# Kernel optimization log

Hardware: AMD Instinct MI355X
Metric: run time of the kernel (lower is better)

## Reference

```python
import jax, jax.numpy as jnp
import numpy as np

B, S, D, C = 64, 576, 768, 200


def setup_inputs() -> dict:
    key = jax.random.key(0)
    k1, k2, k3, k4 = jax.random.split(key, 4)
    return {
        "patch_tokens": jax.random.normal(k1, (B, S, D), dtype=jnp.float32),
        "class_token": jax.random.normal(k2, (B, D), dtype=jnp.float32),
        "attn_w": jax.random.normal(k3, (C, D), dtype=jnp.float32) * (1.0 / np.sqrt(D)),
        "attn_b": jnp.zeros((C,), dtype=jnp.float32),
        "gc_w": jax.random.normal(k4, (C, D), dtype=jnp.float32) * (1.0 / np.sqrt(D)),
        "gc_b": jnp.zeros((C,), dtype=jnp.float32),
        "lam": jnp.ones((1,), dtype=jnp.float32),
    }


def reference(patch_tokens, class_token, attn_w, attn_b, gc_w, gc_b, lam):
    # patch_tokens: (B,S,D). The torch module reshapes S to HxW, but the mean
    # over (H,W) equals the mean over S, so we stay in token layout.
    _, S_, D_ = patch_tokens.shape
    # Global classifier: (B,C)
    global_scores = class_token @ gc_w.T + gc_b
    # Per-class 1x1 conv == per-class linear projection over tokens: (B,C,S)
    att = jax.nn.sigmoid(
        jnp.einsum("bsd,cd->bcs", patch_tokens, attn_w) + attn_b[None, :, None]
    )
    # mean over spatial (S) then mean over channels (D):
    # mean_d mean_s (att * feat) == einsum / (S*D)
    attention_scores = jnp.einsum("bcs,bsd->bc", att, patch_tokens) / (S_ * D_)
    return global_scores + lam[0] * attention_scores
```

## Files before the change

kernel.cpp:

```cpp
#include <hip/hip_runtime.h>
#include <math.h>

#define Bsz  64
#define Ssz  576
#define Dsz  768
#define Csz  200
#define NPAD 208
#define MT   48
#define BK   64
#define NKT  12

typedef float f32x4 __attribute__((ext_vector_type(4)));

#define AS_GLOBAL __attribute__((address_space(1)))
#define AS_LDS    __attribute__((address_space(3)))

__device__ inline void gload16(const void* g, void* l) {
    __builtin_amdgcn_global_load_lds((const AS_GLOBAL unsigned int*)g,
                                     (AS_LDS unsigned int*)l, 16, 0, 0);
}

__global__ __launch_bounds__(256) void prep_w8(const float* __restrict__ W,
                                               unsigned int* __restrict__ Wq) {
    const int i   = blockIdx.x * 256 + threadIdx.x;
    const int row = i / 192;
    const int col = (i % 192) * 4;
    unsigned int w = 0;
    if (row < Csz) {
        const float4 v = *(const float4*)(W + (size_t)row * Dsz + col);
        w = __builtin_amdgcn_cvt_pk_fp8_f32(v.x, v.y, 0u, false);
        w = __builtin_amdgcn_cvt_pk_fp8_f32(v.z, v.w, w, true);
    } else if (row == Csz) {
        w = 0x38383838u;
    }
    Wq[i] = w;
}

__global__ __launch_bounds__(256) void gc_kernel(
    const float* __restrict__ ct, const float* __restrict__ gw,
    const float* __restrict__ gb, float* __restrict__ out) {
    const int b    = blockIdx.x;
    const int wv   = threadIdx.x >> 6;
    const int lane = threadIdx.x & 63;
    const int c    = blockIdx.y * 4 + wv;
    const float* wr = gw + (size_t)c * Dsz + lane * 12;
    const float* cr = ct + (size_t)b * Dsz + lane * 12;
    float s = 0.f;
#pragma unroll
    for (int j = 0; j < 3; ++j) {
        const float4 w = *(const float4*)(wr + 4 * j);
        const float4 x = *(const float4*)(cr + 4 * j);
        s += w.x * x.x + w.y * x.y + w.z * x.z + w.w * x.w;
    }
#pragma unroll
    for (int off = 32; off > 0; off >>= 1) s += __shfl_down(s, off, 64);
    if (lane == 0) out[b * Csz + c] = s + gb[c];
}

__global__ __launch_bounds__(256, 3) void attn_kernel(
    const float* __restrict__ X,
    const unsigned char* __restrict__ Wq,
    const float* __restrict__ attn_b,
    const float* __restrict__ lam,
    float* __restrict__ out)
{
    __shared__ float         sX[2][MT * BK];
    __shared__ unsigned char sW[2][NPAD * BK];

    const int tid  = threadIdx.x;
    const int lane = tid & 63;
    const int w    = tid >> 6;
    const int m    = lane & 15;
    const int q    = lane >> 4;
    const int rowbase = blockIdx.x * MT;
    const int bidx    = blockIdx.x / 12;

    const float* xg[3];
    int xsl[3];
#pragma unroll
    for (int j = 0; j < 3; ++j) {
        const int g    = 3 * w + j;
        const int xrow = g * 4 + (lane >> 4);
        const int xgc  = (lane & 15) ^ (xrow & 15);
        xg[j]  = X + (size_t)(rowbase + xrow) * Dsz + xgc * 4;
        xsl[j] = g * 64;
    }

    const int wng = (w < 3) ? 3 : 4;
    const int wg0 = 3 * w;
    const unsigned char* wgp = Wq + (size_t)(lane >> 2) * Dsz
                                  + (((lane & 3) ^ ((lane >> 2) & 3)) * 16);

    f32x4 acc[13];
#pragma unroll
    for (int t = 0; t < 13; ++t) acc[t] = (f32x4){0.f, 0.f, 0.f, 0.f};

    const int rA   = w * 16 + m;
    const int akey = rA & 15;
    const int bkey = m & 3;

#pragma unroll
    for (int j = 0; j < 3; ++j)
        gload16(xg[j], &sX[0][xsl[j] * 4]);
#pragma unroll
    for (int j = 0; j < 4; ++j)
        if (j < wng) gload16(wgp + (size_t)(wg0 + j) * 16 * Dsz, &sW[0][(wg0 + j) * 1024]);

    for (int kt = 0; kt < NKT; ++kt) {
        const int p = kt & 1;
        __syncthreads();
        if (kt + 1 < NKT) {
            const int kx = (kt + 1) * BK;
#pragma unroll
            for (int j = 0; j < 3; ++j)
                gload16(xg[j] + kx, &sX[p ^ 1][xsl[j] * 4]);
#pragma unroll
            for (int j = 0; j < 4; ++j)
                if (j < wng) gload16(wgp + (size_t)(wg0 + j) * 16 * Dsz + kx,
                                     &sW[p ^ 1][(wg0 + j) * 1024]);
        }
        if (w < 3) {
#pragma unroll
            for (int k2 = 0; k2 < 2; ++k2) {
                const int c0 = k2 * 8 + 2 * q;
                const float4 alo = *(const float4*)&sX[p][rA * 64 + ((c0) ^ akey) * 4];
                const float4 ahi = *(const float4*)&sX[p][rA * 64 + ((c0 + 1) ^ akey) * 4];
                union { long l; unsigned int u[2]; } A;
                A.u[0] = __builtin_amdgcn_cvt_pk_fp8_f32(alo.x, alo.y, 0u, false);
                A.u[0] = __builtin_amdgcn_cvt_pk_fp8_f32(alo.z, alo.w, A.u[0], true);
                A.u[1] = __builtin_amdgcn_cvt_pk_fp8_f32(ahi.x, ahi.y, 0u, false);
                A.u[1] = __builtin_amdgcn_cvt_pk_fp8_f32(ahi.z, ahi.w, A.u[1], true);
                const unsigned char* wb =
                    &sW[p][m * 64 + ((k2 * 2 + (q >> 1)) ^ bkey) * 16 + (q & 1) * 8];
#pragma unroll
                for (int t = 0; t < 13; ++t) {
                    const long B = *(const long*)(wb + t * 1024);
                    acc[t] = __builtin_amdgcn_mfma_f32_16x16x32_fp8_fp8(A.l, B, acc[t], 0, 0, 0);
                }
            }
        }
    }

    if (w < 3) {
        float rsv[4];
#pragma unroll
        for (int r = 0; r < 4; ++r) rsv[r] = __shfl(acc[12][r], (lane & 48) + 8, 64);

        const float scale = lam[0] * (1.f / ((float)Ssz * (float)Dsz));
#pragma unroll
        for (int t = 0; t < 13; ++t) {
            const int c = t * 16 + m;
            if (c < Csz) {
                const float bias = attn_b[c];
                float s = 0.f;
#pragma unroll
                for (int r = 0; r < 4; ++r)
                    s += rsv[r] / (1.f + __expf(-(acc[t][r] + bias)));
                s += __shfl_xor(s, 16, 64);
                s += __shfl_xor(s, 32, 64);
                if (q == 0) atomicAdd(&out[bidx * Csz + c], s * scale);
            }
        }
    }
}

extern "C" void kernel_launch(void* const* d_in, const int* in_sizes, int n_in,
                              void* d_out, int out_size, void* d_ws, size_t ws_size,
                              hipStream_t stream) {
    const float* X   = (const float*)d_in[0];
    const float* ct  = (const float*)d_in[1];
    const float* aw  = (const float*)d_in[2];
    const float* ab  = (const float*)d_in[3];
    const float* gw  = (const float*)d_in[4];
    const float* gb  = (const float*)d_in[5];
    const float* lam = (const float*)d_in[6];
    float* out = (float*)d_out;
    unsigned char* Wq = (unsigned char*)d_ws;

    prep_w8<<<(NPAD * Dsz / 4) / 256, 256, 0, stream>>>(aw, (unsigned int*)Wq);
    gc_kernel<<<dim3(Bsz, Csz / 4), 256, 0, stream>>>(ct, gw, gb, out);
    attn_kernel<<<(Bsz * Ssz) / MT, 256, 0, stream>>>(X, Wq, ab, lam, out);
}
```

Measured before the change: 197.5 us.

## Stage full fp8 weight in LDS once and stream X via registers

The attention kernel now loads the entire fp8 weight matrix (208x768) into LDS once per block and drops the per-k-tile double-buffered LDS staging of X and W. Each wave reads its X rows straight from global memory into registers with a four-slot prefetch ring, and the loader-only fourth wave is removed by launching 192 threads. This is meant to remove the per-tile barriers and the X round trip through LDS. In exchange it needs about 160KB of LDS and many more registers, which limits occupancy to one block per CU and exposes the initial weight load latency.

```diff
diff --git a/kernel.cpp b/kernel.cpp
--- a/kernel.cpp
+++ b/kernel.cpp
@@ -7,8 +7,8 @@
 #define Csz  200
 #define NPAD 208
 #define MT   48
-#define BK   64
 #define NKT  12
+#define NCH  48
 
 typedef float f32x4 __attribute__((ext_vector_type(4)));
 
@@ -57,15 +57,14 @@
     if (lane == 0) out[b * Csz + c] = s + gb[c];
 }
 
-__global__ __launch_bounds__(256, 3) void attn_kernel(
+__global__ __launch_bounds__(192, 1) void attn_kernel(
     const float* __restrict__ X,
     const unsigned char* __restrict__ Wq,
     const float* __restrict__ attn_b,
     const float* __restrict__ lam,
     float* __restrict__ out)
 {
-    __shared__ float         sX[2][MT * BK];
-    __shared__ unsigned char sW[2][NPAD * BK];
+    __shared__ unsigned char sW[NPAD * NCH * 16];
 
     const int tid  = threadIdx.x;
     const int lane = tid & 63;
@@ -75,91 +74,76 @@
     const int rowbase = blockIdx.x * MT;
     const int bidx    = blockIdx.x / 12;
 
-    const float* xg[3];
-    int xsl[3];
+    const float* xp = X + (size_t)(rowbase + w * 16 + m) * Dsz + q * 8;
+
+    f32x4 xa[4][4];
 #pragma unroll
-    for (int j = 0; j < 3; ++j) {
-        const int g    = 3 * w + j;
-        const int xrow = g * 4 + (lane >> 4);
-        const int xgc  = (lane & 15) ^ (xrow & 15);
-        xg[j]  = X + (size_t)(rowbase + xrow) * Dsz + xgc * 4;
-        xsl[j] = g * 64;
+    for (int kt = 0; kt < 4; ++kt) {
+#pragma unroll
+        for (int j = 0; j < 4; ++j)
+            xa[kt][j] = *(const f32x4*)(xp + kt * 64 + (j >> 1) * 32 + (j & 1) * 4);
     }
 
-    const int wng = (w < 3) ? 3 : 4;
-    const int wg0 = 3 * w;
-    const unsigned char* wgp = Wq + (size_t)(lane >> 2) * Dsz
-                                  + (((lane & 3) ^ ((lane >> 2) & 3)) * 16);
+#pragma unroll 4
+    for (int j = 0; j < 52; ++j) {
+        const int g = w * 52 + j;
+        const int s = g * 64 + lane;
+        const int c = s / NPAD;
+        const int r = s - c * NPAD;
+        gload16(Wq + (size_t)r * Dsz + c * 16, &sW[(size_t)(g * 64) * 16]);
+    }
 
     f32x4 acc[13];
 #pragma unroll
     for (int t = 0; t < 13; ++t) acc[t] = (f32x4){0.f, 0.f, 0.f, 0.f};
 
-    const int rA   = w * 16 + m;
-    const int akey = rA & 15;
-    const int bkey = m & 3;
+    const int wbase = m * 16 + (q & 1) * 8 + (q >> 1) * 3328;
+
+    __syncthreads();
 
 #pragma unroll
-    for (int j = 0; j < 3; ++j)
-        gload16(xg[j], &sX[0][xsl[j] * 4]);
+    for (int kt = 0; kt < NKT; ++kt) {
+        const int slot = kt & 3;
 #pragma unroll
-    for (int j = 0; j < 4; ++j)
-        if (j < wng) gload16(wgp + (size_t)(wg0 + j) * 16 * Dsz, &sW[0][(wg0 + j) * 1024]);
-
-    for (int kt = 0; kt < NKT; ++kt) {
-        const int p = kt & 1;
-        __syncthreads();
-        if (kt + 1 < NKT) {
-            const int kx = (kt + 1) * BK;
+        for (int k2 = 0; k2 < 2; ++k2) {
+            const f32x4 alo = xa[slot][k2 * 2];
+            const f32x4 ahi = xa[slot][k2 * 2 + 1];
+            union { long l; unsigned int u[2]; } A;
+            A.u[0] = __builtin_amdgcn_cvt_pk_fp8_f32(alo.x, alo.y, 0u, false);
+            A.u[0] = __builtin_amdgcn_cvt_pk_fp8_f32(alo.z, alo.w, A.u[0], true);
+            A.u[1] = __builtin_amdgcn_cvt_pk_fp8_f32(ahi.x, ahi.y, 0u, false);
+            A.u[1] = __builtin_amdgcn_cvt_pk_fp8_f32(ahi.z, ahi.w, A.u[1], true);
+            const unsigned char* wb = &sW[(kt * 4 + k2 * 2) * 3328 + wbase];
 #pragma unroll
-            for (int j = 0; j < 3; ++j)
-                gload16(xg[j] + kx, &sX[p ^ 1][xsl[j] * 4]);
+            for (int t = 0; t < 13; ++t) {
+                const long Bf = *(const long*)(wb + t * 256);
+                acc[t] = __builtin_amdgcn_mfma_f32_16x16x32_fp8_fp8(A.l, Bf, acc[t], 0, 0, 0);
+            }
+        }
+        if (kt + 4 < NKT) {
 #pragma unroll
             for (int j = 0; j < 4; ++j)
-                if (j < wng) gload16(wgp + (size_t)(wg0 + j) * 16 * Dsz + kx,
-                                     &sW[p ^ 1][(wg0 + j) * 1024]);
-        }
-        if (w < 3) {
-#pragma unroll
-            for (int k2 = 0; k2 < 2; ++k2) {
-                const int c0 = k2 * 8 + 2 * q;
-                const float4 alo = *(const float4*)&sX[p][rA * 64 + ((c0) ^ akey) * 4];
-                const float4 ahi = *(const float4*)&sX[p][rA * 64 + ((c0 + 1) ^ akey) * 4];
-                union { long l; unsigned int u[2]; } A;
-                A.u[0] = __builtin_amdgcn_cvt_pk_fp8_f32(alo.x, alo.y, 0u, false);
-                A.u[0] = __builtin_amdgcn_cvt_pk_fp8_f32(alo.z, alo.w, A.u[0], true);
-                A.u[1] = __builtin_amdgcn_cvt_pk_fp8_f32(ahi.x, ahi.y, 0u, false);
-                A.u[1] = __builtin_amdgcn_cvt_pk_fp8_f32(ahi.z, ahi.w, A.u[1], true);
-                const unsigned char* wb =
-                    &sW[p][m * 64 + ((k2 * 2 + (q >> 1)) ^ bkey) * 16 + (q & 1) * 8];
-#pragma unroll
-                for (int t = 0; t < 13; ++t) {
-                    const long B = *(const long*)(wb + t * 1024);
-                    acc[t] = __builtin_amdgcn_mfma_f32_16x16x32_fp8_fp8(A.l, B, acc[t], 0, 0, 0);
-                }
-            }
+                xa[slot][j] = *(const f32x4*)(xp + (kt + 4) * 64 + (j >> 1) * 32 + (j & 1) * 4);
         }
     }
 
-    if (w < 3) {
-        float rsv[4];
+    float rsv[4];
 #pragma unroll
-        for (int r = 0; r < 4; ++r) rsv[r] = __shfl(acc[12][r], (lane & 48) + 8, 64);
+    for (int r = 0; r < 4; ++r) rsv[r] = __shfl(acc[12][r], (lane & 48) + 8, 64);
 
-        const float scale = lam[0] * (1.f / ((float)Ssz * (float)Dsz));
+    const float scale = lam[0] * (1.f / ((float)Ssz * (float)Dsz));
 #pragma unroll
-        for (int t = 0; t < 13; ++t) {
-            const int c = t * 16 + m;
-            if (c < Csz) {
-                const float bias = attn_b[c];
-                float s = 0.f;
+    for (int t = 0; t < 13; ++t) {
+        const int c = t * 16 + m;
+        if (c < Csz) {
+            const float bias = attn_b[c];
+            float s = 0.f;
 #pragma unroll
-                for (int r = 0; r < 4; ++r)
-                    s += rsv[r] / (1.f + __expf(-(acc[t][r] + bias)));
-                s += __shfl_xor(s, 16, 64);
-                s += __shfl_xor(s, 32, 64);
-                if (q == 0) atomicAdd(&out[bidx * Csz + c], s * scale);
-            }
+            for (int r = 0; r < 4; ++r)
+                s += rsv[r] / (1.f + __expf(-(acc[t][r] + bias)));
+            s += __shfl_xor(s, 16, 64);
+            s += __shfl_xor(s, 32, 64);
+            if (q == 0) atomicAdd(&out[bidx * Csz + c], s * scale);
         }
     }
 }
@@ -179,5 +163,5 @@
 
     prep_w8<<<(NPAD * Dsz / 4) / 256, 256, 0, stream>>>(aw, (unsigned int*)Wq);
     gc_kernel<<<dim3(Bsz, Csz / 4), 256, 0, stream>>>(ct, gw, gb, out);
-    attn_kernel<<<(Bsz * Ssz) / MT, 256, 0, stream>>>(X, Wq, ab, lam, out);
+    attn_kernel<<<(Bsz * Ssz) / MT, 192, 0, stream>>>(X, Wq, ab, lam, out);
 }
```

New measurement: 240.0 us. 1.22x slower.
